# Performance work log

Measured on AMD Instinct MI355X. Metric: run time of the kernel, lower is better.

## Reference

```python
import jax, jax.numpy as jnp
import numpy as np

H = 64  # hidden_size
I = 8   # input_size
O = 1   # output_size


def setup_inputs() -> dict:
    key = jax.random.key(0)
    ks = jax.random.split(key, 7)
    B, T = 4096, 512
    s_ih = 1.0 / np.sqrt(H)
    inp = {
        "x": jax.random.normal(ks[0], (B, T, I), dtype=jnp.float32),
        # PyTorch LSTM params: W_ih [4H, I], W_hh [4H, H], biases [4H] (gate order i,f,g,o)
        "W_ih": jax.random.uniform(ks[1], (4 * H, I), jnp.float32, -s_ih, s_ih),
        "W_hh": jax.random.uniform(ks[2], (4 * H, H), jnp.float32, -s_ih, s_ih),
        "b_ih": jax.random.uniform(ks[3], (4 * H,), jnp.float32, -s_ih, s_ih),
        "b_hh": jax.random.uniform(ks[4], (4 * H,), jnp.float32, -s_ih, s_ih),
        "W_fc": jax.random.uniform(ks[5], (O, H), jnp.float32, -s_ih, s_ih),
        "b_fc": jax.random.uniform(ks[6], (O,), jnp.float32, -s_ih, s_ih),
    }
    return inp


def _lstm_last_h(x, W_ih, W_hh, b_ih, b_hh):
    B, T, _ = x.shape
    # Precompute input contributions for all timesteps: [T, B, 4H]
    xg = jnp.einsum("bti,gi->tbg", x, W_ih) + (b_ih + b_hh)

    def step(carry, xg_t):
        h, c = carry
        gates = xg_t + h @ W_hh.T  # [B, 4H]
        i, f, g, o = jnp.split(gates, 4, axis=-1)  # torch gate order i,f,g,o
        i = jax.nn.sigmoid(i)
        f = jax.nn.sigmoid(f)
        g = jnp.tanh(g)
        o = jax.nn.sigmoid(o)
        c = f * c + i * g
        h = o * jnp.tanh(c)
        return (h, c), None

    h0 = jnp.zeros((B, H), x.dtype)
    c0 = jnp.zeros((B, H), x.dtype)
    (h_T, _), _ = jax.lax.scan(step, (h0, c0), xg)
    return h_T  # [B, H] == out[:, -1, :]


def reference(x, W_ih, W_hh, b_ih, b_hh, W_fc, b_fc):
    h_T = _lstm_last_h(x, W_ih, W_hh, b_ih, b_hh)
    return h_T @ W_fc.T + b_fc  # [B, O]
```

## Files before the change

kernel.cpp:

```cpp
#include <hip/hip_runtime.h>

#define HSZ 64
#define ISZ 8
#define TSZ 512
#define BTILE 8
#define NW 8
#define KP 104

typedef _Float16 f16;
typedef __attribute__((ext_vector_type(8))) _Float16 f16x8;
typedef __attribute__((ext_vector_type(4))) float f32x4;
typedef unsigned short u16;

__device__ __forceinline__ u16 f16bits(float f) {
    union { f16 h; u16 u; } v; v.h = (f16)f;
    return v.u;
}

__global__ __launch_bounds__(512, 4) void lstm_dual(
    const float* __restrict__ x,
    const float* __restrict__ W_ih,
    const float* __restrict__ W_hh,
    const float* __restrict__ b_ih,
    const float* __restrict__ b_hh,
    const float* __restrict__ W_fc,
    const float* __restrict__ b_fc,
    float* __restrict__ out)
{
    const int tid = threadIdx.x;
    const int w  = tid >> 6;
    const int l  = tid & 63;
    const int lr = l & 15;
    const int lg = l >> 4;
    const int B0 = blockIdx.x * BTILE;

    __shared__ __align__(16) u16 H[2][16][KP];
    __shared__ float red[NW][16];

    for (int i = tid; i < 2 * 16 * KP; i += 512)
        ((u16*)H)[i] = 0;

    const int gate = lr & 3;
    const float sc = (gate == 2) ? -2.885390082f : -1.442695041f;
    f16x8 wa0[2], wa1[2], wa2[2];
    f32x4 bias4[2];
#pragma unroll
    for (int q = 0; q < 2; ++q) {
        const int n  = 2 * w + q;
        const int gc = gate * HSZ + 4 * n + (lr >> 2);
        {
            const float4 a = *reinterpret_cast<const float4*>(&W_hh[gc * HSZ + lg * 8]);
            const float4 b = *reinterpret_cast<const float4*>(&W_hh[gc * HSZ + lg * 8 + 4]);
            wa0[q][0] = (f16)(sc * a.x); wa0[q][1] = (f16)(sc * a.y);
            wa0[q][2] = (f16)(sc * a.z); wa0[q][3] = (f16)(sc * a.w);
            wa0[q][4] = (f16)(sc * b.x); wa0[q][5] = (f16)(sc * b.y);
            wa0[q][6] = (f16)(sc * b.z); wa0[q][7] = (f16)(sc * b.w);
        }
        {
            const float4 a = *reinterpret_cast<const float4*>(&W_hh[gc * HSZ + 32 + lg * 8]);
            const float4 b = *reinterpret_cast<const float4*>(&W_hh[gc * HSZ + 32 + lg * 8 + 4]);
            wa1[q][0] = (f16)(sc * a.x); wa1[q][1] = (f16)(sc * a.y);
            wa1[q][2] = (f16)(sc * a.z); wa1[q][3] = (f16)(sc * a.w);
            wa1[q][4] = (f16)(sc * b.x); wa1[q][5] = (f16)(sc * b.y);
            wa1[q][6] = (f16)(sc * b.z); wa1[q][7] = (f16)(sc * b.w);
        }
#pragma unroll
        for (int j = 0; j < 8; ++j) wa2[q][j] = (f16)0.0f;
        if (lg == 0) {
            const float4 a = *reinterpret_cast<const float4*>(&W_ih[gc * ISZ]);
            const float4 b = *reinterpret_cast<const float4*>(&W_ih[gc * ISZ + 4]);
            wa2[q][0] = (f16)(sc * a.x); wa2[q][1] = (f16)(sc * a.y);
            wa2[q][2] = (f16)(sc * a.z); wa2[q][3] = (f16)(sc * a.w);
            wa2[q][4] = (f16)(sc * b.x); wa2[q][5] = (f16)(sc * b.y);
            wa2[q][6] = (f16)(sc * b.z); wa2[q][7] = (f16)(sc * b.w);
        }
        const int hc = 4 * n + lg;
#pragma unroll
        for (int r = 0; r < 4; ++r) {
            const float s = (r == 2) ? -2.885390082f : -1.442695041f;
            bias4[q][r] = s * (b_ih[r * HSZ + hc] + b_hh[r * HSZ + hc]);
        }
    }

    __syncthreads();

    const float* xptr = x + (size_t)(B0 + (l >> 3)) * TSZ * ISZ + (l & 7);
    if (w == 0)
        H[0][l >> 3][HSZ + (l & 7)] = f16bits(xptr[0]);
    __syncthreads();

    const u16* rd0 = &H[0][lr][lg * 8];
    const u16* rd1 = &H[1][lr][lg * 8];
    const int hcol0 = 8 * w + lg, hcol1 = 8 * w + 4 + lg;
    u16* wrA0 = &H[0][lr][hcol0];  u16* wrA1 = &H[0][lr][hcol1];
    u16* wrB0 = &H[1][lr][hcol0];  u16* wrB1 = &H[1][lr][hcol1];
    u16* xsA  = &H[0][l >> 3][HSZ + (l & 7)];
    u16* xsB  = &H[1][l >> 3][HSZ + (l & 7)];

    float c0 = 0.f, c1 = 0.f, h0 = 0.f, h1 = 0.f;
    const float L2 = 2.885390082f;

#define ACT(ACC, CC, HH)                                                       \
    {                                                                          \
        const float ea = __builtin_amdgcn_exp2f((ACC)[0]);                     \
        const float eb = __builtin_amdgcn_exp2f((ACC)[1]);                     \
        const float ed = __builtin_amdgcn_exp2f((ACC)[2]);                     \
        const float es = __builtin_amdgcn_exp2f((ACC)[3]);                     \
        const float A1 = 1.0f + ea, B1 = 1.0f + eb, D1 = 1.0f + ed;            \
        const float R1 = __builtin_amdgcn_rcpf(A1 * B1 * D1);                  \
        CC = fmaf(CC * A1, D1, (1.0f - ed) * B1) * R1;                         \
        const float eu = __builtin_amdgcn_exp2f(-L2 * CC);                     \
        const float R2 = __builtin_amdgcn_rcpf((1.0f + es) * (1.0f + eu));     \
        HH = (1.0f - eu) * R2;                                                 \
    }

#define STEP(RD, WR0, WR1, XS, XIDX, XGUARD)                                   \
    {                                                                          \
        float xv = 0.0f;                                                       \
        if ((w == 0) && (XGUARD))                                              \
            xv = xptr[(size_t)(XIDX) * ISZ];                                   \
        const f16x8 b0 = *reinterpret_cast<const f16x8*>(RD);                  \
        const f16x8 b1 = *reinterpret_cast<const f16x8*>(RD + 32);             \
        f16x8 b2 = {};                                                         \
        if (lg == 0)                                                           \
            b2 = *reinterpret_cast<const f16x8*>(RD + 64);                     \
        f32x4 a0 = __builtin_amdgcn_mfma_f32_16x16x32_f16(wa2[0], b2, bias4[0], 0, 0, 0); \
        f32x4 a1 = __builtin_amdgcn_mfma_f32_16x16x32_f16(wa2[1], b2, bias4[1], 0, 0, 0); \
        a0 = __builtin_amdgcn_mfma_f32_16x16x32_f16(wa0[0], b0, a0, 0, 0, 0);  \
        a1 = __builtin_amdgcn_mfma_f32_16x16x32_f16(wa0[1], b0, a1, 0, 0, 0);  \
        a0 = __builtin_amdgcn_mfma_f32_16x16x32_f16(wa1[0], b1, a0, 0, 0, 0);  \
        a1 = __builtin_amdgcn_mfma_f32_16x16x32_f16(wa1[1], b1, a1, 0, 0, 0);  \
        ACT(a0, c0, h0)                                                        \
        ACT(a1, c1, h1)                                                        \
        *(WR0) = f16bits(h0);                                                  \
        *(WR1) = f16bits(h1);                                                  \
        if ((w == 0) && (XGUARD))                                              \
            *(XS) = f16bits(xv);                                               \
        __syncthreads();                                                       \
    }

    for (int t = 0; t < TSZ; t += 2) {
        STEP(rd0, wrB0, wrB1, xsB, t + 1, true)
        STEP(rd1, wrA0, wrA1, xsA, t + 2, t < TSZ - 2)
    }
#undef STEP
#undef ACT

    float v = h0 * W_fc[hcol0] + h1 * W_fc[hcol1];
    v += __shfl_xor(v, 16);
    v += __shfl_xor(v, 32);
    if (lg == 0) red[w][lr] = v;
    __syncthreads();
    if (tid < BTILE) {
        float s = b_fc[0];
#pragma unroll
        for (int ww = 0; ww < NW; ++ww) s += red[ww][tid];
        out[B0 + tid] = s;
    }
}

extern "C" void kernel_launch(void* const* d_in, const int* in_sizes, int n_in,
                              void* d_out, int out_size, void* d_ws, size_t ws_size,
                              hipStream_t stream) {
    const float* x    = (const float*)d_in[0];
    const float* W_ih = (const float*)d_in[1];
    const float* W_hh = (const float*)d_in[2];
    const float* b_ih = (const float*)d_in[3];
    const float* b_hh = (const float*)d_in[4];
    const float* W_fc = (const float*)d_in[5];
    const float* b_fc = (const float*)d_in[6];
    float* out = (float*)d_out;

    const int B = in_sizes[0] / (TSZ * ISZ);
    lstm_dual<<<B / BTILE, NW * 64, 0, stream>>>(x, W_ih, W_hh, b_ih, b_hh, W_fc, b_fc, out);
}
```

Before: 315.2 us.

## Fill all 16 MFMA batch columns and feed x from registers into MFMA operand

The batch tile per block goes from 8 to 16, so every column of the 16x16 MFMA output now holds a real sequence instead of half being padding, and the grid is halved. Each lane now loads its own x row with float4 loads straight into registers and builds the input-projection B operand there. This removes the shared-memory staging of x and its guarded single-element loads. The hidden-unit mapping is changed so each lane writes its two h values as one packed 32-bit LDS store, and the padded LDS row width shrinks. The trade-off is fewer blocks and a different occupancy, since the launch-bounds minimum of 4 blocks is dropped, plus redundant per-lane x loads.

```diff
diff --git a/kernel.cpp b/kernel.cpp
--- a/kernel.cpp
+++ b/kernel.cpp
@@ -3,21 +3,22 @@
 #define HSZ 64
 #define ISZ 8
 #define TSZ 512
-#define BTILE 8
+#define BTILE 16
 #define NW 8
-#define KP 104
+#define KP 72
 
 typedef _Float16 f16;
 typedef __attribute__((ext_vector_type(8))) _Float16 f16x8;
 typedef __attribute__((ext_vector_type(4))) float f32x4;
 typedef unsigned short u16;
+typedef unsigned int u32;
 
 __device__ __forceinline__ u16 f16bits(float f) {
     union { f16 h; u16 u; } v; v.h = (f16)f;
     return v.u;
 }
 
-__global__ __launch_bounds__(512, 4) void lstm_dual(
+__global__ __launch_bounds__(512) void lstm_gx(
     const float* __restrict__ x,
     const float* __restrict__ W_ih,
     const float* __restrict__ W_hh,
@@ -34,20 +35,20 @@
     const int lg = l >> 4;
     const int B0 = blockIdx.x * BTILE;
 
-    __shared__ __align__(16) u16 H[2][16][KP];
-    __shared__ float red[NW][16];
+    __shared__ __align__(16) u16 H[2][BTILE][KP];
+    __shared__ float red[NW][BTILE];
 
-    for (int i = tid; i < 2 * 16 * KP; i += 512)
-        ((u16*)H)[i] = 0;
+    for (int i = tid; i < 2 * BTILE * KP / 2; i += 512)
+        ((u32*)H)[i] = 0;
 
     const int gate = lr & 3;
+    const int slot = lr >> 2;
     const float sc = (gate == 2) ? -2.885390082f : -1.442695041f;
     f16x8 wa0[2], wa1[2], wa2[2];
     f32x4 bias4[2];
 #pragma unroll
     for (int q = 0; q < 2; ++q) {
-        const int n  = 2 * w + q;
-        const int gc = gate * HSZ + 4 * n + (lr >> 2);
+        const int gc = gate * HSZ + 8 * w + 2 * slot + q;
         {
             const float4 a = *reinterpret_cast<const float4*>(&W_hh[gc * HSZ + lg * 8]);
             const float4 b = *reinterpret_cast<const float4*>(&W_hh[gc * HSZ + lg * 8 + 4]);
@@ -74,30 +75,26 @@
             wa2[q][4] = (f16)(sc * b.x); wa2[q][5] = (f16)(sc * b.y);
             wa2[q][6] = (f16)(sc * b.z); wa2[q][7] = (f16)(sc * b.w);
         }
-        const int hc = 4 * n + lg;
+        const int hq = 8 * w + 2 * lg + q;
 #pragma unroll
         for (int r = 0; r < 4; ++r) {
             const float s = (r == 2) ? -2.885390082f : -1.442695041f;
-            bias4[q][r] = s * (b_ih[r * HSZ + hc] + b_hh[r * HSZ + hc]);
+            bias4[q][r] = s * (b_ih[r * HSZ + hq] + b_hh[r * HSZ + hq]);
         }
     }
 
     __syncthreads();
 
-    const float* xptr = x + (size_t)(B0 + (l >> 3)) * TSZ * ISZ + (l & 7);
-    if (w == 0)
-        H[0][l >> 3][HSZ + (l & 7)] = f16bits(xptr[0]);
-    __syncthreads();
-
     const u16* rd0 = &H[0][lr][lg * 8];
     const u16* rd1 = &H[1][lr][lg * 8];
-    const int hcol0 = 8 * w + lg, hcol1 = 8 * w + 4 + lg;
-    u16* wrA0 = &H[0][lr][hcol0];  u16* wrA1 = &H[0][lr][hcol1];
-    u16* wrB0 = &H[1][lr][hcol0];  u16* wrB1 = &H[1][lr][hcol1];
-    u16* xsA  = &H[0][l >> 3][HSZ + (l & 7)];
-    u16* xsB  = &H[1][l >> 3][HSZ + (l & 7)];
+    u32* wr0 = (u32*)&H[0][lr][8 * w + 2 * lg];
+    u32* wr1 = (u32*)&H[1][lr][8 * w + 2 * lg];
 
-    float c0 = 0.f, c1 = 0.f, h0 = 0.f, h1 = 0.f;
+    const float* xrow = x + (size_t)(B0 + lr) * TSZ * ISZ;
+    float4 xa = *reinterpret_cast<const float4*>(xrow);
+    float4 xb = *reinterpret_cast<const float4*>(xrow + 4);
+
+    float c0 = 0.f, h0 = 0.f, c1 = 0.f, h1 = 0.f;
     const float L2 = 2.885390082f;
 
 #define ACT(ACC, CC, HH)                                                       \
@@ -114,16 +111,18 @@
         HH = (1.0f - eu) * R2;                                                 \
     }
 
-#define STEP(RD, WR0, WR1, XS, XIDX, XGUARD)                                   \
+#define STEP(RD, WR, T, GUARD)                                                 \
     {                                                                          \
-        float xv = 0.0f;                                                       \
-        if ((w == 0) && (XGUARD))                                              \
-            xv = xptr[(size_t)(XIDX) * ISZ];                                   \
+        f16x8 b2;                                                              \
+        b2[0] = (f16)xa.x; b2[1] = (f16)xa.y; b2[2] = (f16)xa.z;               \
+        b2[3] = (f16)xa.w; b2[4] = (f16)xb.x; b2[5] = (f16)xb.y;               \
+        b2[6] = (f16)xb.z; b2[7] = (f16)xb.w;                                  \
+        if (GUARD) {               \
+            xa = *reinterpret_cast<const float4*>(xrow + (size_t)(T + 1) * ISZ);     \
+            xb = *reinterpret_cast<const float4*>(xrow + (size_t)(T + 1) * ISZ + 4); \
+        }                                                                      \
         const f16x8 b0 = *reinterpret_cast<const f16x8*>(RD);                  \
         const f16x8 b1 = *reinterpret_cast<const f16x8*>(RD + 32);             \
-        f16x8 b2 = {};                                                         \
-        if (lg == 0)                                                           \
-            b2 = *reinterpret_cast<const f16x8*>(RD + 64);                     \
         f32x4 a0 = __builtin_amdgcn_mfma_f32_16x16x32_f16(wa2[0], b2, bias4[0], 0, 0, 0); \
         f32x4 a1 = __builtin_amdgcn_mfma_f32_16x16x32_f16(wa2[1], b2, bias4[1], 0, 0, 0); \
         a0 = __builtin_amdgcn_mfma_f32_16x16x32_f16(wa0[0], b0, a0, 0, 0, 0);  \
@@ -132,24 +131,22 @@
         a1 = __builtin_amdgcn_mfma_f32_16x16x32_f16(wa1[1], b1, a1, 0, 0, 0);  \
         ACT(a0, c0, h0)                                                        \
         ACT(a1, c1, h1)                                                        \
-        *(WR0) = f16bits(h0);                                                  \
-        *(WR1) = f16bits(h1);                                                  \
-        if ((w == 0) && (XGUARD))                                              \
-            *(XS) = f16bits(xv);                                               \
+        *(WR) = (u32)f16bits(h0) | ((u32)f16bits(h1) << 16);                   \
         __syncthreads();                                                       \
     }
 
     for (int t = 0; t < TSZ; t += 2) {
-        STEP(rd0, wrB0, wrB1, xsB, t + 1, true)
-        STEP(rd1, wrA0, wrA1, xsA, t + 2, t < TSZ - 2)
+        STEP(rd0, wr1, t, true)
+        STEP(rd1, wr0, t + 1, t < TSZ - 2)
     }
 #undef STEP
 #undef ACT
 
-    float v = h0 * W_fc[hcol0] + h1 * W_fc[hcol1];
+    const int hc = 8 * w + 2 * lg;
+    float v = fmaf(h0, W_fc[hc], h1 * W_fc[hc + 1]);
     v += __shfl_xor(v, 16);
     v += __shfl_xor(v, 32);
-    if (lg == 0) red[w][lr] = v;
+    if (l < 16) red[w][lr] = v;
     __syncthreads();
     if (tid < BTILE) {
         float s = b_fc[0];
@@ -172,5 +169,5 @@
     float* out = (float*)d_out;
 
     const int B = in_sizes[0] / (TSZ * ISZ);
-    lstm_dual<<<B / BTILE, NW * 64, 0, stream>>>(x, W_ih, W_hh, b_ih, b_hh, W_fc, b_fc, out);
+    lstm_gx<<<B / BTILE, NW * 64, 0, stream>>>(x, W_ih, W_hh, b_ih, b_hh, W_fc, b_fc, out);
 }
```

After: 286.8 us. -9.0%, faster.
